# Performance work log

Measured on AMD Instinct MI355X. Metric: run time of the kernel, lower is better.

Reference implementation:

```python
import jax, jax.numpy as jnp
import numpy as np

EMB = 256
ENT_NUM = 100000
REL_NUM = 2000
B = 512


def setup_inputs() -> dict:
    key = jax.random.key(0)
    ks = jax.random.split(key, 10)
    s = 0.02
    return {
        "left_child": jax.random.normal(ks[0], (B, 3, EMB), jnp.float32),
        "right_child": jax.random.normal(ks[1], (B, 3, EMB), jnp.float32),
        "query": jax.random.normal(ks[2], (B, 3, EMB), jnp.float32),
        "ent_emb": jax.random.normal(ks[3], (ENT_NUM, EMB), jnp.float32) * s,
        "rel_emb": jax.random.normal(ks[4], (REL_NUM, EMB), jnp.float32) * s,
        "W_left": jax.random.normal(ks[5], (EMB, EMB), jnp.float32) * s,
        "b_left": jnp.zeros((EMB,), jnp.float32),
        "W_right": jax.random.normal(ks[6], (EMB, EMB), jnp.float32) * s,
        "b_right": jnp.zeros((EMB,), jnp.float32),
        "W_ent": jax.random.normal(ks[7], (EMB, 3 * EMB), jnp.float32) * s,
        "b_ent": jnp.zeros((EMB,), jnp.float32),
    }


def _attend(q, table):
    # q: [B, E], table: [N, E]. Fused form of expand*mul*sum + softmax + expand*mul*sum.
    logits = q @ table.T                     # [B, N]
    probs = jax.nn.softmax(logits, axis=1)   # [B, N]
    return probs @ table                     # [B, E]


def reference(left_child, right_child, query, ent_emb, rel_emb,
              W_left, b_left, W_right, b_right, W_ent, b_ent):
    q1 = query[:, 1, :]
    left_rel = q1 @ W_left.T + b_left
    right_rel = q1 @ W_right.T + b_right
    # cat(query[:,0], query[:,1], query[:,2]) along dim 1 == reshape
    q_cat = query.reshape(query.shape[0], 3 * EMB)
    q_ent = q_cat @ W_ent.T + b_ent

    o_ent = _attend(q_ent, ent_emb)
    o_left_r = _attend(left_rel, rel_emb)
    o_right_r = _attend(right_rel, rel_emb)

    new_left = jnp.stack([left_child[:, 0, :], o_left_r, o_ent], axis=1)
    new_right = jnp.stack([o_ent, o_right_r, right_child[:, 2, :]], axis=1)
    return (new_left, new_right)
```

## Files before the change

kernel.cpp:

```cpp
#include <hip/hip_runtime.h>
#include <hip/hip_bf16.h>
#include <math.h>

typedef __bf16 bf16;
typedef unsigned short u16;
typedef unsigned int u32;
typedef unsigned long long u64;
typedef long long i64;
typedef unsigned char u8;
typedef __attribute__((ext_vector_type(8))) __bf16 bf16x8;
typedef __attribute__((ext_vector_type(16))) float f32x16;
typedef __attribute__((ext_vector_type(8))) int i32x8;
typedef __attribute__((address_space(1))) void gvoid;
typedef __attribute__((address_space(3))) void svoid;

#define ENT_N 100000
#define REL_N 2000
#define ENT_CH 120
#define REL_CH 4

static __device__ __forceinline__ i32x8 mk8(uint4 a, uint4 b) {
    i32x8 r;
    r[0] = (int)a.x; r[1] = (int)a.y; r[2] = (int)a.z; r[3] = (int)a.w;
    r[4] = (int)b.x; r[5] = (int)b.y; r[6] = (int)b.z; r[7] = (int)b.w;
    return r;
}

__global__ __launch_bounds__(256) void prep_copy(
    const float* __restrict__ query,
    const float* __restrict__ W_left, const float* __restrict__ b_left,
    const float* __restrict__ W_right, const float* __restrict__ b_right,
    const float* __restrict__ W_ent, const float* __restrict__ b_ent,
    const float* __restrict__ lc, const float* __restrict__ rc,
    bf16* __restrict__ qe, bf16* __restrict__ ql, bf16* __restrict__ qr,
    u8* __restrict__ qe8, u8* __restrict__ ql8, u8* __restrict__ qr8,
    float* __restrict__ out)
{
    __shared__ float qs[4 * 768];
    const int t = threadIdx.x;
    if (blockIdx.x >= 128) {
        const int idx = (blockIdx.x - 128) * 256 + t;
        if (idx < 32768) {
            const int q = idx >> 6, e4 = idx & 63;
            float4 v = *(const float4*)(lc + (size_t)q * 768 + e4 * 4);
            *(float4*)(out + (size_t)q * 768 + e4 * 4) = v;
        } else {
            const int j = idx - 32768;
            const int q = j >> 6, e4 = j & 63;
            float4 v = *(const float4*)(rc + (size_t)q * 768 + 512 + e4 * 4);
            *(float4*)(out + (size_t)393216 + q * 768 + 512 + e4 * 4) = v;
        }
        return;
    }
    const int b0 = blockIdx.x * 4;
#pragma unroll
    for (int i = 0; i < 12; ++i)
        qs[t + 256 * i] = query[(size_t)b0 * 768 + t + 256 * i];
    __syncthreads();

    const int j = t;
    float ae[4], al[4], ar[4];
    const float be = b_ent[j], bl = b_left[j], br = b_right[j];
#pragma unroll
    for (int r = 0; r < 4; ++r) { ae[r] = be; al[r] = bl; ar[r] = br; }

    const float* we = W_ent + (size_t)j * 768;
    for (int k = 0; k < 768; k += 4) {
        const float4 wv = *(const float4*)(we + k);
#pragma unroll
        for (int r = 0; r < 4; ++r) {
            const float* qq = qs + r * 768 + k;
            ae[r] += wv.x * qq[0] + wv.y * qq[1] + wv.z * qq[2] + wv.w * qq[3];
        }
    }
    const float* wl = W_left + (size_t)j * 256;
    const float* wr = W_right + (size_t)j * 256;
    for (int k = 0; k < 256; k += 4) {
        const float4 w1 = *(const float4*)(wl + k);
        const float4 w2 = *(const float4*)(wr + k);
#pragma unroll
        for (int r = 0; r < 4; ++r) {
            const float* qq = qs + r * 768 + 256 + k;
            al[r] += w1.x * qq[0] + w1.y * qq[1] + w1.z * qq[2] + w1.w * qq[3];
            ar[r] += w2.x * qq[0] + w2.y * qq[1] + w2.z * qq[2] + w2.w * qq[3];
        }
    }
#pragma unroll
    for (int r = 0; r < 4; ++r) {
        qe[(size_t)(b0 + r) * 256 + j] = (bf16)ae[r];
        ql[(size_t)(b0 + r) * 256 + j] = (bf16)al[r];
        qr[(size_t)(b0 + r) * 256 + j] = (bf16)ar[r];
        qe8[(size_t)(b0 + r) * 256 + j] =
            (u8)__builtin_amdgcn_cvt_pk_fp8_f32(ae[r], ae[r], 0, false);
        ql8[(size_t)(b0 + r) * 256 + j] =
            (u8)__builtin_amdgcn_cvt_pk_fp8_f32(al[r], al[r], 0, false);
        qr8[(size_t)(b0 + r) * 256 + j] =
            (u8)__builtin_amdgcn_cvt_pk_fp8_f32(ar[r], ar[r], 0, false);
    }
}

__global__ __launch_bounds__(256) void conv_fused(
    const float* __restrict__ entF, const float* __restrict__ relF,
    u8* __restrict__ entT, u8* __restrict__ entB,
    u8* __restrict__ relT, u8* __restrict__ relB)
{
    const float* in; u8* outT; u8* outB; int R; int g;
    if (blockIdx.x < 1563) {
        in = entF; outT = entT; outB = entB; R = ENT_N; g = blockIdx.x;
    } else {
        in = relF; outT = relT; outB = relB; R = REL_N; g = blockIdx.x - 1563;
    }
    const int r0 = g * 64;
    __shared__ float tile[64 * 65];
    const int t = threadIdx.x;
    const int e0 = blockIdx.y * 64;

    const int eg = t & 7, rowb = t >> 3;
#pragma unroll
    for (int item = 0; item < 2; ++item) {
        const int r = rowb + item * 32;
        float4 a, b;
        if ((r0 + r) < R) {
            const float* src = in + (size_t)(r0 + r) * 256 + e0 + eg * 8;
            a = *(const float4*)src;
            b = *(const float4*)(src + 4);
        } else { a = make_float4(0.f, 0.f, 0.f, 0.f); b = a; }
        float* dst = tile + r * 65 + eg * 8;
        dst[0] = a.x; dst[1] = a.y; dst[2] = a.z; dst[3] = a.w;
        dst[4] = b.x; dst[5] = b.y; dst[6] = b.z; dst[7] = b.w;
    }
    __syncthreads();

    {
        const int n2 = t >> 2, piece = t & 3;
        const int sub = n2 >> 5, nn = n2 & 31;
        const int kbk = piece >> 1, jh = piece & 1;
        const float* src = tile + n2 * 65 + kbk * 32 + jh * 16;
        u32 x; uint4 o;
        x = __builtin_amdgcn_cvt_pk_fp8_f32(src[0], src[1], 0, false);
        o.x = __builtin_amdgcn_cvt_pk_fp8_f32(src[2], src[3], x, true);
        x = __builtin_amdgcn_cvt_pk_fp8_f32(src[4], src[5], 0, false);
        o.y = __builtin_amdgcn_cvt_pk_fp8_f32(src[6], src[7], x, true);
        x = __builtin_amdgcn_cvt_pk_fp8_f32(src[8], src[9], 0, false);
        o.z = __builtin_amdgcn_cvt_pk_fp8_f32(src[10], src[11], x, true);
        x = __builtin_amdgcn_cvt_pk_fp8_f32(src[12], src[13], 0, false);
        o.w = __builtin_amdgcn_cvt_pk_fp8_f32(src[14], src[15], x, true);
        *(uint4*)(outB + (size_t)g * 16384 + sub * 8192 +
                  (size_t)blockIdx.y * 2048 + kbk * 1024 + nn * 32 + jh * 16) = o;
    }
    {
        const int etl = t >> 7, kbv = (t >> 6) & 1;
        const int nv = (t >> 1) & 31, jh = t & 1;
        const int colL = etl * 32 + nv;
        float v[16];
#pragma unroll
        for (int i = 0; i < 16; ++i) {
            const int row = jh * 32 + (i & 3) + 8 * (i >> 2) + 4 * kbv;
            v[i] = tile[row * 65 + colL];
        }
        u32 x; uint4 o;
        x = __builtin_amdgcn_cvt_pk_fp8_f32(v[0], v[1], 0, false);
        o.x = __builtin_amdgcn_cvt_pk_fp8_f32(v[2], v[3], x, true);
        x = __builtin_amdgcn_cvt_pk_fp8_f32(v[4], v[5], 0, false);
        o.y = __builtin_amdgcn_cvt_pk_fp8_f32(v[6], v[7], x, true);
        x = __builtin_amdgcn_cvt_pk_fp8_f32(v[8], v[9], 0, false);
        o.z = __builtin_amdgcn_cvt_pk_fp8_f32(v[10], v[11], x, true);
        x = __builtin_amdgcn_cvt_pk_fp8_f32(v[12], v[13], 0, false);
        o.w = __builtin_amdgcn_cvt_pk_fp8_f32(v[14], v[15], x, true);
        *(uint4*)(outT + (size_t)g * 16384 +
                  (size_t)(blockIdx.y * 2 + etl) * 2048 +
                  kbv * 1024 + nv * 32 + jh * 16) = o;
    }
}

__global__ __launch_bounds__(256, 2) void flash10(
    const u8* __restrict__ qeP, const u8* __restrict__ qlP,
    const u8* __restrict__ qrP,
    const u8* __restrict__ entB, const u8* __restrict__ relB,
    const u8* __restrict__ entT, const u8* __restrict__ relT,
    float* __restrict__ entL, float* __restrict__ relLL,
    float* __restrict__ relLR,
    u16* __restrict__ entO, u16* __restrict__ relOL, u16* __restrict__ relOR)
{
    const int tid = threadIdx.x;
    const int w = tid >> 6;
    const int lane = tid & 63;
    const int n = lane & 31;
    const int kb = lane >> 5;

    int qt, c, stride, nt, Nrows;
    const u8* qbf; const u8* tabB; const u8* tabT;
    float* pL; u16* pO;
    {
        const int id = blockIdx.x;
        if (id < 480) {
            qt = id / 120; c = id % 120;
            stride = 120; nt = (c < 3) ? 14 : 13;
            Nrows = ENT_N;
            qbf = qeP; tabB = entB; tabT = entT; pL = entL; pO = entO;
        } else {
            const int r = id - 480;
            qt = (r >> 2) & 3; c = r & 3;
            stride = 4; nt = 8;
            Nrows = REL_N;
            tabB = relB; tabT = relT;
            if (r < 16) { qbf = qlP; pL = relLL; pO = relOL; }
            else        { qbf = qrP; pL = relLR; pO = relOR; }
        }
    }
    const int q0 = qt * 128;
    const int qw = q0 + w * 32;

    __shared__ __align__(16) u8 lds[65536];
    u16* lds16 = (u16*)lds;

    const u8* qrow = qbf + (size_t)(qw + n) * 256;
    i32x8 qf[4];
#pragma unroll
    for (int kc = 0; kc < 4; ++kc) {
        uint4 a = *(const uint4*)(qrow + kc * 64 + kb * 32);
        uint4 b = *(const uint4*)(qrow + kc * 64 + kb * 32 + 16);
        qf[kc] = mk8(a, b);
    }

    f32x16 acc[8];
#pragma unroll
    for (int et = 0; et < 8; ++et)
#pragma unroll
        for (int i = 0; i < 16; ++i) acc[et][i] = 0.f;
    float l_run = 0.f;

    auto stage = [&](int buf, int g) {
        u8* sK = lds + buf * 32768;
        u8* sV = sK + 16384;
        const u8* ksrc = tabB + (size_t)g * 16384 + w * 4096 + (size_t)lane * 16;
        const u8* vsrc = tabT + (size_t)g * 16384 + w * 4096 + (size_t)lane * 16;
#pragma unroll
        for (int o = 0; o < 4096; o += 1024) {
            __builtin_amdgcn_global_load_lds((gvoid*)(ksrc + o),
                                             (svoid*)(sK + w * 4096 + o), 16, 0, 0);
            __builtin_amdgcn_global_load_lds((gvoid*)(vsrc + o),
                                             (svoid*)(sV + w * 4096 + o), 16, 0, 0);
        }
    };

    int rt = c;
    stage(0, rt);
    __syncthreads();

    for (int k = 0; k < nt; ++k) {
        if (k + 1 < nt) stage((k + 1) & 1, rt + stride);

        const u8* sK = lds + (k & 1) * 32768;
        const u8* sV = sK + 16384;
        const int gr = rt * 64;

        f32x16 L0, L1;
#pragma unroll
        for (int i = 0; i < 16; ++i) { L0[i] = 0.f; L1[i] = 0.f; }
        const u8* kbase = sK + kb * 1024 + n * 32;
#pragma unroll
        for (int kc = 0; kc < 4; ++kc) {
            uint4 a0 = *(const uint4*)(kbase + kc * 2048);
            uint4 a1 = *(const uint4*)(kbase + kc * 2048 + 16);
            L0 = __builtin_amdgcn_mfma_scale_f32_32x32x64_f8f6f4(
                mk8(a0, a1), qf[kc], L0, 0, 0, 0, 0x7f7f7f7f, 0, 0x7f7f7f7f);
            uint4 b0 = *(const uint4*)(kbase + 8192 + kc * 2048);
            uint4 b1 = *(const uint4*)(kbase + 8192 + kc * 2048 + 16);
            L1 = __builtin_amdgcn_mfma_scale_f32_32x32x64_f8f6f4(
                mk8(b0, b1), qf[kc], L1, 0, 0, 0, 0x7f7f7f7f, 0, 0x7f7f7f7f);
        }
        if (gr + 64 > Nrows) {
#pragma unroll
            for (int r = 0; r < 16; ++r) {
                const int row = (r & 3) + 8 * (r >> 2) + 4 * kb;
                if (gr + row >= Nrows)      L0[r] = -1e30f;
                if (gr + 32 + row >= Nrows) L1[r] = -1e30f;
            }
        }
        float rs = 0.f;
#pragma unroll
        for (int r = 0; r < 16; ++r) {
            const float p0 = __expf(L0[r]); L0[r] = p0; rs += p0;
            const float p1 = __expf(L1[r]); L1[r] = p1; rs += p1;
        }
        rs += __shfl_xor(rs, 32);
        l_run += rs;
        u32 p[8];
#pragma unroll
        for (int i = 0; i < 4; ++i) {
            u32 x = __builtin_amdgcn_cvt_pk_fp8_f32(L0[i * 4 + 0], L0[i * 4 + 1], 0, false);
            p[i] = __builtin_amdgcn_cvt_pk_fp8_f32(L0[i * 4 + 2], L0[i * 4 + 3], x, true);
            u32 y = __builtin_amdgcn_cvt_pk_fp8_f32(L1[i * 4 + 0], L1[i * 4 + 1], 0, false);
            p[i + 4] = __builtin_amdgcn_cvt_pk_fp8_f32(L1[i * 4 + 2], L1[i * 4 + 3], y, true);
        }
        uint4 pa; pa.x = p[0]; pa.y = p[1]; pa.z = p[2]; pa.w = p[3];
        uint4 pb; pb.x = p[4]; pb.y = p[5]; pb.z = p[6]; pb.w = p[7];
        const i32x8 bv = mk8(pa, pb);
        const u8* vbase = sV + kb * 1024 + n * 32;
#pragma unroll
        for (int et = 0; et < 8; ++et) {
            uint4 v0 = *(const uint4*)(vbase + et * 2048);
            uint4 v1 = *(const uint4*)(vbase + et * 2048 + 16);
            acc[et] = __builtin_amdgcn_mfma_scale_f32_32x32x64_f8f6f4(
                mk8(v0, v1), bv, acc[et], 0, 0, 0, 0x7f7f7f7f, 0, 0x7f7f7f7f);
        }
        rt += stride;
        __syncthreads();
    }

    if (lane < 32) pL[(size_t)c * 512 + qw + n] = l_run;

    for (int half = 0; half < 2; ++half) {
        __syncthreads();
        if ((w >> 1) == half) {
            u16* rgn = lds16 + (w & 1) * 8448;
#pragma unroll
            for (int et = 0; et < 8; ++et)
#pragma unroll
                for (int a2 = 0; a2 < 4; ++a2) {
                    bf16 h0 = (bf16)acc[et][a2 * 4 + 0];
                    bf16 h1 = (bf16)acc[et][a2 * 4 + 1];
                    bf16 h2 = (bf16)acc[et][a2 * 4 + 2];
                    bf16 h3 = (bf16)acc[et][a2 * 4 + 3];
                    uint2 pk;
                    pk.x = ((u32)(*(u16*)&h1) << 16) | (u32)(*(u16*)&h0);
                    pk.y = ((u32)(*(u16*)&h3) << 16) | (u32)(*(u16*)&h2);
                    *(uint2*)(rgn + n * 264 + et * 32 + 8 * a2 + 4 * kb) = pk;
                }
        }
        __syncthreads();
#pragma unroll
        for (int rg = 0; rg < 2; ++rg) {
            const int qt2 = q0 + (half * 2 + rg) * 32;
            const u16* src = lds16 + rg * 8448;
            const int qq = tid >> 3, e0 = (tid & 7) * 32;
#pragma unroll
            for (int i = 0; i < 4; ++i) {
                const u16* sp = src + qq * 264 + e0 + i * 8;
                uint2 a = *(const uint2*)(sp);
                uint2 b = *(const uint2*)(sp + 4);
                uint4 wv; wv.x = a.x; wv.y = a.y; wv.z = b.x; wv.w = b.y;
                *(uint4*)(pO + ((size_t)c * 512 + qt2 + qq) * 256 + e0 + i * 8) = wv;
            }
        }
    }
}

__global__ __launch_bounds__(256) void combine_all(
    const u16* __restrict__ entO, const float* __restrict__ entL,
    const u16* __restrict__ relOL, const float* __restrict__ relLL,
    const u16* __restrict__ relOR, const float* __restrict__ relLR,
    float* __restrict__ out)
{
    const u16* pO; const float* pl; int CH, baseA, baseB;
    if (blockIdx.y == 0) { pO = entO; pl = entL; CH = ENT_CH; baseA = 512; baseB = 393216; }
    else if (blockIdx.y == 1) { pO = relOL; pl = relLL; CH = REL_CH; baseA = 256; baseB = -1; }
    else { pO = relOR; pl = relLR; CH = REL_CH; baseA = 393472; baseB = -1; }

    const int idx = blockIdx.x * 256 + threadIdx.x;
    const int q = idx >> 5;
    const int e0 = (idx & 31) * 8;
    float s = 0.f;
#pragma unroll 4
    for (int c = 0; c < CH; ++c) s += pl[(size_t)c * 512 + q];
    const float inv = 1.f / s;
    float a[8];
#pragma unroll
    for (int k = 0; k < 8; ++k) a[k] = 0.f;
#pragma unroll 4
    for (int c = 0; c < CH; ++c) {
        const uint4 wv = *(const uint4*)(pO + ((size_t)c * 512 + q) * 256 + e0);
        const u32 ww[4] = {wv.x, wv.y, wv.z, wv.w};
#pragma unroll
        for (int p = 0; p < 4; ++p) {
            a[p * 2]     += __uint_as_float((ww[p] & 0xffffu) << 16);
            a[p * 2 + 1] += __uint_as_float(ww[p] & 0xffff0000u);
        }
    }
#pragma unroll
    for (int k = 0; k < 8; ++k) a[k] *= inv;
    float4 o1 = {a[0], a[1], a[2], a[3]};
    float4 o2 = {a[4], a[5], a[6], a[7]};
    *(float4*)(out + (size_t)baseA + (size_t)q * 768 + e0) = o1;
    *(float4*)(out + (size_t)baseA + (size_t)q * 768 + e0 + 4) = o2;
    if (baseB >= 0) {
        *(float4*)(out + (size_t)baseB + (size_t)q * 768 + e0) = o1;
        *(float4*)(out + (size_t)baseB + (size_t)q * 768 + e0 + 4) = o2;
    }
}

__global__ __launch_bounds__(256) void attend_simple(
    const bf16* __restrict__ qbf, const float* __restrict__ tab, int Nrows,
    float* __restrict__ out, int baseA, int baseB)
{
    const int q = blockIdx.x;
    const int t = threadIdx.x, wave = t >> 6, lane = t & 63;
    float qv[4];
#pragma unroll
    for (int i = 0; i < 4; ++i) qv[i] = (float)qbf[(size_t)q * 256 + lane + 64 * i];
    float m = -INFINITY, l = 0.f, o[4] = {0.f, 0.f, 0.f, 0.f};
    for (int r = wave; r < Nrows; r += 4) {
        const float* row = tab + (size_t)r * 256;
        float d = 0.f;
#pragma unroll
        for (int i = 0; i < 4; ++i) d += qv[i] * row[lane + 64 * i];
#pragma unroll
        for (int s = 32; s; s >>= 1) d += __shfl_xor(d, s);
        const float mn = fmaxf(m, d);
        const float al = __expf(m - mn);
        const float p = __expf(d - mn);
#pragma unroll
        for (int i = 0; i < 4; ++i) o[i] = o[i] * al + p * row[lane + 64 * i];
        l = l * al + p; m = mn;
    }
    __shared__ float sm[4], sl[4], so[4][256];
    if (lane == 0) { sm[wave] = m; sl[wave] = l; }
#pragma unroll
    for (int i = 0; i < 4; ++i) so[wave][lane + 64 * i] = o[i];
    __syncthreads();
    const float M = fmaxf(fmaxf(sm[0], sm[1]), fmaxf(sm[2], sm[3]));
    const float w0 = __expf(sm[0] - M), w1 = __expf(sm[1] - M);
    const float w2 = __expf(sm[2] - M), w3 = __expf(sm[3] - M);
    const float L = w0 * sl[0] + w1 * sl[1] + w2 * sl[2] + w3 * sl[3];
    const float a = (w0 * so[0][t] + w1 * so[1][t] + w2 * so[2][t] + w3 * so[3][t]) / L;
    out[(size_t)baseA + (size_t)q * 768 + t] = a;
    if (baseB >= 0) out[(size_t)baseB + (size_t)q * 768 + t] = a;
}

extern "C" void kernel_launch(void* const* d_in, const int* in_sizes, int n_in,
                              void* d_out, int out_size, void* d_ws, size_t ws_size,
                              hipStream_t stream)
{
    const float* left_child  = (const float*)d_in[0];
    const float* right_child = (const float*)d_in[1];
    const float* query       = (const float*)d_in[2];
    const float* ent_emb     = (const float*)d_in[3];
    const float* rel_emb     = (const float*)d_in[4];
    const float* W_left      = (const float*)d_in[5];
    const float* b_left      = (const float*)d_in[6];
    const float* W_right     = (const float*)d_in[7];
    const float* b_right     = (const float*)d_in[8];
    const float* W_ent       = (const float*)d_in[9];
    const float* b_ent       = (const float*)d_in[10];
    float* out = (float*)d_out;
    char* ws = (char*)d_ws;

    bf16* qe_bf = (bf16*)(ws + 0);
    bf16* ql_bf = (bf16*)(ws + 262144);
    bf16* qr_bf = (bf16*)(ws + 524288);
    u8*   qe8   = (u8*)(ws + 786432);
    u8*   ql8   = (u8*)(ws + 917504);
    u8*   qr8   = (u8*)(ws + 1048576);
    u8*   entT8 = (u8*)(ws + 1179648);
    u8*   relT8 = (u8*)(ws + 26787840);
    u8*   entB8 = (u8*)(ws + 27312128);
    u8*   relB8 = (u8*)(ws + 52920320);
    float* entL = (float*)(ws + 53444608);
    u16*  entO  = (u16*)(ws + 53690368);
    float* relLL = (float*)(ws + 85147648);
    float* relLR = (float*)(ws + 85155840);
    u16*  relOL = (u16*)(ws + 85164032);
    u16*  relOR = (u16*)(ws + 86212608);
    const size_t WS_FULL = 87261184;
    const size_t WS_FALLBACK = 786432;

    prep_copy<<<dim3(384), dim3(256), 0, stream>>>(
        query, W_left, b_left, W_right, b_right, W_ent, b_ent,
        left_child, right_child, qe_bf, ql_bf, qr_bf, qe8, ql8, qr8, out);

    if (ws_size >= WS_FULL) {
        conv_fused<<<dim3(1595, 4), dim3(256), 0, stream>>>(
            ent_emb, rel_emb, entT8, entB8, relT8, relB8);
        flash10<<<dim3(512), dim3(256), 0, stream>>>(
            qe8, ql8, qr8, entB8, relB8, entT8, relT8,
            entL, relLL, relLR, entO, relOL, relOR);
        combine_all<<<dim3(64, 3), dim3(256), 0, stream>>>(
            entO, entL, relOL, relLL, relOR, relLR, out);
    } else if (ws_size >= WS_FALLBACK) {
        attend_simple<<<dim3(512), dim3(256), 0, stream>>>(qe_bf, ent_emb, ENT_N, out, 512, 393216);
        attend_simple<<<dim3(512), dim3(256), 0, stream>>>(ql_bf, rel_emb, REL_N, out, 256, -1);
        attend_simple<<<dim3(512), dim3(256), 0, stream>>>(qr_bf, rel_emb, REL_N, out, 393472, -1);
    }
    (void)in_sizes; (void)n_in; (void)out_size;
}
```

Before: 289.9 us.

## Fuse projection prep, embedding fp8 conversion and child copy into one launch

Merges the projection/prep kernel and the embedding fp8 conversion kernel into a single launch whose block index picks the role. The projection is re-tiled from 128 blocks into 1536 smaller blocks, each computing 64 output columns for 4 rows with weights staged through shared memory, so the work spreads across many more CUs. This removes one kernel launch boundary and lets the small projection overlap with the bandwidth-bound conversion. In exchange the blocks are heterogeneous and each one reserves the larger shared-memory footprint.

```diff
diff --git a/kernel.cpp b/kernel.cpp
--- a/kernel.cpp
+++ b/kernel.cpp
@@ -19,6 +19,10 @@
 #define ENT_CH 120
 #define REL_CH 4
 
+#define NPREPM 1536
+#define NCONV  6380
+#define NCOPY  256
+
 static __device__ __forceinline__ i32x8 mk8(uint4 a, uint4 b) {
     i32x8 r;
     r[0] = (int)a.x; r[1] = (int)a.y; r[2] = (int)a.z; r[3] = (int)a.w;
@@ -26,7 +30,51 @@
     return r;
 }
 
-__global__ __launch_bounds__(256) void prep_copy(
+template<int KLEN>
+static __device__ __forceinline__ void prep_tile(
+    const float* __restrict__ query, const float* __restrict__ W,
+    const float* __restrict__ bias, int b0, int rowbase, int qwoff,
+    bf16* __restrict__ outBf, u8* __restrict__ out8, float* smem)
+{
+    const int t = threadIdx.x;
+    float* qs = smem;
+    float* Wl = smem + 4 * KLEN;
+
+#pragma unroll
+    for (int i = 0; i < 4 * KLEN / 256; ++i) {
+        const int l = t + 256 * i;
+        const int r = l / KLEN, k = l % KLEN;
+        qs[l] = query[(size_t)(b0 + r) * 768 + qwoff + k];
+    }
+
+    const int j = t & 63, r = t >> 6;
+    float acc = 0.f;
+    const float* wbase = W + (size_t)rowbase * KLEN;
+
+    for (int c = 0; c < KLEN / 32; ++c) {
+        __syncthreads();
+#pragma unroll
+        for (int p = 0; p < 2; ++p) {
+            const int idx = t + p * 256;
+            const int row = idx >> 3, kq = idx & 7;
+            const float4 v = *(const float4*)(wbase + (size_t)row * KLEN + c * 32 + kq * 4);
+            float* d = Wl + row * 33 + kq * 4;
+            d[0] = v.x; d[1] = v.y; d[2] = v.z; d[3] = v.w;
+        }
+        __syncthreads();
+        const float* wr = Wl + j * 33;
+        const float* qr = qs + r * KLEN + c * 32;
+#pragma unroll
+        for (int k = 0; k < 32; ++k) acc += wr[k] * qr[k];
+    }
+    acc += bias[rowbase + j];
+
+    const size_t o = (size_t)(b0 + r) * 256 + rowbase + j;
+    outBf[o] = (bf16)acc;
+    out8[o] = (u8)__builtin_amdgcn_cvt_pk_fp8_f32(acc, acc, 0, false);
+}
+
+__global__ __launch_bounds__(256) void prep_conv(
     const float* __restrict__ query,
     const float* __restrict__ W_left, const float* __restrict__ b_left,
     const float* __restrict__ W_right, const float* __restrict__ b_right,
@@ -34,12 +82,30 @@
     const float* __restrict__ lc, const float* __restrict__ rc,
     bf16* __restrict__ qe, bf16* __restrict__ ql, bf16* __restrict__ qr,
     u8* __restrict__ qe8, u8* __restrict__ ql8, u8* __restrict__ qr8,
-    float* __restrict__ out)
+    float* __restrict__ out,
+    const float* __restrict__ entF, const float* __restrict__ relF,
+    u8* __restrict__ entT, u8* __restrict__ entB,
+    u8* __restrict__ relT, u8* __restrict__ relB,
+    int nconv)
 {
-    __shared__ float qs[4 * 768];
+    __shared__ float smem[5184];
+    const int blk = blockIdx.x;
     const int t = threadIdx.x;
-    if (blockIdx.x >= 128) {
-        const int idx = (blockIdx.x - 128) * 256 + t;
+
+    if (blk < NPREPM) {
+        const int rg = blk / 12, jt = blk % 12;
+        const int b0 = rg * 4;
+        const int proj = jt >> 2, rowbase = (jt & 3) * 64;
+        if (proj == 0)
+            prep_tile<768>(query, W_ent, b_ent, b0, rowbase, 0, qe, qe8, smem);
+        else if (proj == 1)
+            prep_tile<256>(query, W_left, b_left, b0, rowbase, 256, ql, ql8, smem);
+        else
+            prep_tile<256>(query, W_right, b_right, b0, rowbase, 256, qr, qr8, smem);
+        return;
+    }
+    if (blk >= NPREPM + nconv) {
+        const int idx = (blk - NPREPM - nconv) * 256 + t;
         if (idx < 32768) {
             const int q = idx >> 6, e4 = idx & 63;
             float4 v = *(const float4*)(lc + (size_t)q * 768 + e4 * 4);
@@ -52,68 +118,18 @@
         }
         return;
     }
-    const int b0 = blockIdx.x * 4;
-#pragma unroll
-    for (int i = 0; i < 12; ++i)
-        qs[t + 256 * i] = query[(size_t)b0 * 768 + t + 256 * i];
-    __syncthreads();
-
-    const int j = t;
-    float ae[4], al[4], ar[4];
-    const float be = b_ent[j], bl = b_left[j], br = b_right[j];
-#pragma unroll
-    for (int r = 0; r < 4; ++r) { ae[r] = be; al[r] = bl; ar[r] = br; }
-
-    const float* we = W_ent + (size_t)j * 768;
-    for (int k = 0; k < 768; k += 4) {
-        const float4 wv = *(const float4*)(we + k);
-#pragma unroll
-        for (int r = 0; r < 4; ++r) {
-            const float* qq = qs + r * 768 + k;
-            ae[r] += wv.x * qq[0] + wv.y * qq[1] + wv.z * qq[2] + wv.w * qq[3];
-        }
-    }
-    const float* wl = W_left + (size_t)j * 256;
-    const float* wr = W_right + (size_t)j * 256;
-    for (int k = 0; k < 256; k += 4) {
-        const float4 w1 = *(const float4*)(wl + k);
-        const float4 w2 = *(const float4*)(wr + k);
-#pragma unroll
-        for (int r = 0; r < 4; ++r) {
-            const float* qq = qs + r * 768 + 256 + k;
-            al[r] += w1.x * qq[0] + w1.y * qq[1] + w1.z * qq[2] + w1.w * qq[3];
-            ar[r] += w2.x * qq[0] + w2.y * qq[1] + w2.z * qq[2] + w2.w * qq[3];
-        }
-    }
-#pragma unroll
-    for (int r = 0; r < 4; ++r) {
-        qe[(size_t)(b0 + r) * 256 + j] = (bf16)ae[r];
-        ql[(size_t)(b0 + r) * 256 + j] = (bf16)al[r];
-        qr[(size_t)(b0 + r) * 256 + j] = (bf16)ar[r];
-        qe8[(size_t)(b0 + r) * 256 + j] =
-            (u8)__builtin_amdgcn_cvt_pk_fp8_f32(ae[r], ae[r], 0, false);
-        ql8[(size_t)(b0 + r) * 256 + j] =
-            (u8)__builtin_amdgcn_cvt_pk_fp8_f32(al[r], al[r], 0, false);
-        qr8[(size_t)(b0 + r) * 256 + j] =
-            (u8)__builtin_amdgcn_cvt_pk_fp8_f32(ar[r], ar[r], 0, false);
-    }
-}
-
-__global__ __launch_bounds__(256) void conv_fused(
-    const float* __restrict__ entF, const float* __restrict__ relF,
-    u8* __restrict__ entT, u8* __restrict__ entB,
-    u8* __restrict__ relT, u8* __restrict__ relB)
-{
+
+    const int cidx = blk - NPREPM;
+    const int x = cidx >> 2, y = cidx & 3;
     const float* in; u8* outT; u8* outB; int R; int g;
-    if (blockIdx.x < 1563) {
-        in = entF; outT = entT; outB = entB; R = ENT_N; g = blockIdx.x;
+    if (x < 1563) {
+        in = entF; outT = entT; outB = entB; R = ENT_N; g = x;
     } else {
-        in = relF; outT = relT; outB = relB; R = REL_N; g = blockIdx.x - 1563;
+        in = relF; outT = relT; outB = relB; R = REL_N; g = x - 1563;
     }
     const int r0 = g * 64;
-    __shared__ float tile[64 * 65];
-    const int t = threadIdx.x;
-    const int e0 = blockIdx.y * 64;
+    float* tile = smem;
+    const int e0 = y * 64;
 
     const int eg = t & 7, rowb = t >> 3;
 #pragma unroll
@@ -136,17 +152,17 @@
         const int sub = n2 >> 5, nn = n2 & 31;
         const int kbk = piece >> 1, jh = piece & 1;
         const float* src = tile + n2 * 65 + kbk * 32 + jh * 16;
-        u32 x; uint4 o;
-        x = __builtin_amdgcn_cvt_pk_fp8_f32(src[0], src[1], 0, false);
-        o.x = __builtin_amdgcn_cvt_pk_fp8_f32(src[2], src[3], x, true);
-        x = __builtin_amdgcn_cvt_pk_fp8_f32(src[4], src[5], 0, false);
-        o.y = __builtin_amdgcn_cvt_pk_fp8_f32(src[6], src[7], x, true);
-        x = __builtin_amdgcn_cvt_pk_fp8_f32(src[8], src[9], 0, false);
-        o.z = __builtin_amdgcn_cvt_pk_fp8_f32(src[10], src[11], x, true);
-        x = __builtin_amdgcn_cvt_pk_fp8_f32(src[12], src[13], 0, false);
-        o.w = __builtin_amdgcn_cvt_pk_fp8_f32(src[14], src[15], x, true);
+        u32 xx; uint4 o;
+        xx = __builtin_amdgcn_cvt_pk_fp8_f32(src[0], src[1], 0, false);
+        o.x = __builtin_amdgcn_cvt_pk_fp8_f32(src[2], src[3], xx, true);
+        xx = __builtin_amdgcn_cvt_pk_fp8_f32(src[4], src[5], 0, false);
+        o.y = __builtin_amdgcn_cvt_pk_fp8_f32(src[6], src[7], xx, true);
+        xx = __builtin_amdgcn_cvt_pk_fp8_f32(src[8], src[9], 0, false);
+        o.z = __builtin_amdgcn_cvt_pk_fp8_f32(src[10], src[11], xx, true);
+        xx = __builtin_amdgcn_cvt_pk_fp8_f32(src[12], src[13], 0, false);
+        o.w = __builtin_amdgcn_cvt_pk_fp8_f32(src[14], src[15], xx, true);
         *(uint4*)(outB + (size_t)g * 16384 + sub * 8192 +
-                  (size_t)blockIdx.y * 2048 + kbk * 1024 + nn * 32 + jh * 16) = o;
+                  (size_t)y * 2048 + kbk * 1024 + nn * 32 + jh * 16) = o;
     }
     {
         const int etl = t >> 7, kbv = (t >> 6) & 1;
@@ -158,17 +174,17 @@
             const int row = jh * 32 + (i & 3) + 8 * (i >> 2) + 4 * kbv;
             v[i] = tile[row * 65 + colL];
         }
-        u32 x; uint4 o;
-        x = __builtin_amdgcn_cvt_pk_fp8_f32(v[0], v[1], 0, false);
-        o.x = __builtin_amdgcn_cvt_pk_fp8_f32(v[2], v[3], x, true);
-        x = __builtin_amdgcn_cvt_pk_fp8_f32(v[4], v[5], 0, false);
-        o.y = __builtin_amdgcn_cvt_pk_fp8_f32(v[6], v[7], x, true);
-        x = __builtin_amdgcn_cvt_pk_fp8_f32(v[8], v[9], 0, false);
-        o.z = __builtin_amdgcn_cvt_pk_fp8_f32(v[10], v[11], x, true);
-        x = __builtin_amdgcn_cvt_pk_fp8_f32(v[12], v[13], 0, false);
-        o.w = __builtin_amdgcn_cvt_pk_fp8_f32(v[14], v[15], x, true);
+        u32 xx; uint4 o;
+        xx = __builtin_amdgcn_cvt_pk_fp8_f32(v[0], v[1], 0, false);
+        o.x = __builtin_amdgcn_cvt_pk_fp8_f32(v[2], v[3], xx, true);
+        xx = __builtin_amdgcn_cvt_pk_fp8_f32(v[4], v[5], 0, false);
+        o.y = __builtin_amdgcn_cvt_pk_fp8_f32(v[6], v[7], xx, true);
+        xx = __builtin_amdgcn_cvt_pk_fp8_f32(v[8], v[9], 0, false);
+        o.z = __builtin_amdgcn_cvt_pk_fp8_f32(v[10], v[11], xx, true);
+        xx = __builtin_amdgcn_cvt_pk_fp8_f32(v[12], v[13], 0, false);
+        o.w = __builtin_amdgcn_cvt_pk_fp8_f32(v[14], v[15], xx, true);
         *(uint4*)(outT + (size_t)g * 16384 +
-                  (size_t)(blockIdx.y * 2 + etl) * 2048 +
+                  (size_t)(y * 2 + etl) * 2048 +
                   kbv * 1024 + nv * 32 + jh * 16) = o;
     }
 }
@@ -465,19 +481,21 @@
     const size_t WS_FULL = 87261184;
     const size_t WS_FALLBACK = 786432;
 
-    prep_copy<<<dim3(384), dim3(256), 0, stream>>>(
-        query, W_left, b_left, W_right, b_right, W_ent, b_ent,
-        left_child, right_child, qe_bf, ql_bf, qr_bf, qe8, ql8, qr8, out);
-
     if (ws_size >= WS_FULL) {
-        conv_fused<<<dim3(1595, 4), dim3(256), 0, stream>>>(
-            ent_emb, rel_emb, entT8, entB8, relT8, relB8);
+        prep_conv<<<dim3(NPREPM + NCONV + NCOPY), dim3(256), 0, stream>>>(
+            query, W_left, b_left, W_right, b_right, W_ent, b_ent,
+            left_child, right_child, qe_bf, ql_bf, qr_bf, qe8, ql8, qr8, out,
+            ent_emb, rel_emb, entT8, entB8, relT8, relB8, NCONV);
         flash10<<<dim3(512), dim3(256), 0, stream>>>(
             qe8, ql8, qr8, entB8, relB8, entT8, relT8,
             entL, relLL, relLR, entO, relOL, relOR);
         combine_all<<<dim3(64, 3), dim3(256), 0, stream>>>(
             entO, entL, relOL, relLL, relOR, relLR, out);
     } else if (ws_size >= WS_FALLBACK) {
+        prep_conv<<<dim3(NPREPM + NCOPY), dim3(256), 0, stream>>>(
+            query, W_left, b_left, W_right, b_right, W_ent, b_ent,
+            left_child, right_child, qe_bf, ql_bf, qr_bf, qe8, ql8, qr8, out,
+            ent_emb, rel_emb, (u8*)ws, (u8*)ws, (u8*)ws, (u8*)ws, 0);
         attend_simple<<<dim3(512), dim3(256), 0, stream>>>(qe_bf, ent_emb, ENT_N, out, 512, 393216);
         attend_simple<<<dim3(512), dim3(256), 0, stream>>>(ql_bf, rel_emb, REL_N, out, 256, -1);
         attend_simple<<<dim3(512), dim3(256), 0, stream>>>(qr_bf, rel_emb, REL_N, out, 393472, -1);
```

Result: faster. 246.9 us (-14.8%).
